# Optimization experiments

Hardware: AMD Instinct MI355X
Metric: run time of the kernel (lower is better)

## Reference

```python
import jax, jax.numpy as jnp
import numpy as np

B, T, D, H = 8, 1024, 768, 12
HD = D // H  # head_dim = 64


def setup_inputs() -> dict:
    key = jax.random.key(0)
    ks = jax.random.split(key, 6)
    s = 1.0 / np.sqrt(D)
    return {
        "x": jax.random.normal(ks[0], (B, T, D), dtype=jnp.float32),
        "Wq": jax.random.normal(ks[1], (D, D), dtype=jnp.float32) * s,
        "Wk": jax.random.normal(ks[2], (D, D), dtype=jnp.float32) * s,
        "Wv": jax.random.normal(ks[3], (D, D), dtype=jnp.float32) * s,
        "Wp": jax.random.normal(ks[4], (D, D), dtype=jnp.float32) * s,
        "bp": jnp.zeros((D,), dtype=jnp.float32),
    }


def reference(x, Wq, Wk, Wv, Wp, bp):
    Bx, Tx, Dx = x.shape
    # projections (nn.Linear applies x @ W.T; weights here are stored as [out,in]-equivalent square)
    q = (x @ Wq.T).reshape(Bx, Tx, H, HD).transpose(0, 2, 1, 3)  # [B,H,T,hd]
    k = (x @ Wk.T).reshape(Bx, Tx, H, HD).transpose(0, 2, 1, 3)
    v = (x @ Wv.T).reshape(Bx, Tx, H, HD).transpose(0, 2, 1, 3)
    scores = jnp.einsum("bhqd,bhkd->bhqk", q, k)  # raw QK^T, then mask, then scale (as in source)
    causal = jnp.tril(jnp.ones((Tx, Tx), dtype=bool))
    scores = jnp.where(causal, scores, -jnp.inf)
    weights = jax.nn.softmax(scores / np.sqrt(HD), axis=-1)
    # dropout is identity in eval mode
    ctx = jnp.einsum("bhqk,bhkd->bhqd", weights, v)
    ctx = ctx.transpose(0, 2, 1, 3).reshape(Bx, Tx, Dx)
    return ctx @ Wp.T + bp
```

## Files before the change

### kernel.cpp

```cpp
#include <hip/hip_runtime.h>
#include <hip/hip_bf16.h>
#include <math.h>

#define Bsz 8
#define Tsz 1024
#define Dsz 768
#define Hn  12
#define Msz (Bsz*Tsz)
#define NQT (Tsz/64)

typedef __attribute__((ext_vector_type(8))) short bf16x8_t;
typedef __attribute__((ext_vector_type(4))) float f32x4_t;

__device__ __forceinline__ unsigned short f2bf(float f) {
  unsigned u = __builtin_bit_cast(unsigned, f);
  u += 0x7FFFu + ((u >> 16) & 1u);
  return (unsigned short)(u >> 16);
}

__device__ __forceinline__ unsigned short f2bf_fast(float f) {
  __hip_bfloat16 h = __float2bfloat16(f);
  return __builtin_bit_cast(unsigned short, h);
}

__device__ __forceinline__ void gload16(const void* g, const void* l) {
  __builtin_amdgcn_global_load_lds(
      (const __attribute__((address_space(1))) unsigned int*)g,
      (__attribute__((address_space(3))) unsigned int*)l, 16, 0, 0);
}

#define XBLKS (Msz*Dsz/1024)
#define WBLKS (Dsz*Dsz/1024)
__global__ __launch_bounds__(256) void cvt_all_kernel(
    const float* __restrict__ x,
    const float* __restrict__ w0, const float* __restrict__ w1,
    const float* __restrict__ w2, const float* __restrict__ w3,
    unsigned short* __restrict__ xb,
    unsigned short* __restrict__ o0, unsigned short* __restrict__ o1,
    unsigned short* __restrict__ o2, unsigned short* __restrict__ o3) {
  int bid = blockIdx.x;
  const float* src; unsigned short* dst; size_t blk;
  if (bid < XBLKS) { src = x; dst = xb; blk = bid; }
  else {
    int t = bid - XBLKS;
    int which = t / WBLKS;
    blk = t % WBLKS;
    switch (which) {
      case 0: src = w0; dst = o0; break;
      case 1: src = w1; dst = o1; break;
      case 2: src = w2; dst = o2; break;
      default: src = w3; dst = o3; break;
    }
  }
  size_t idx = (blk * 256 + threadIdx.x) * 4;
  float4 v = *(const float4*)(src + idx);
  union { unsigned short u[4]; uint2 w; } t;
  t.u[0] = f2bf(v.x); t.u[1] = f2bf(v.y); t.u[2] = f2bf(v.z); t.u[3] = f2bf(v.w);
  *(uint2*)(dst + idx) = t.w;
}

__global__ __launch_bounds__(256) void gemm_qkv_kernel(
    const unsigned short* __restrict__ X, const unsigned short* __restrict__ Wcat,
    unsigned short* __restrict__ Yq, unsigned short* __restrict__ Yk,
    unsigned short* __restrict__ Yvt) {
  __shared__ __align__(16) unsigned short As[128 * 64];
  __shared__ __align__(16) unsigned short Bs[128 * 64];
  const int tid = threadIdx.x;
  const int w = tid >> 6, lane = tid & 63;
  const int i = lane & 15, g = lane >> 4;
  const int wr = w >> 1, wc = w & 1;
  const int bm = blockIdx.x * 128, bn = blockIdx.y * 128;
  const int sr = lane >> 3;
  const int scb = ((lane & 7) * 16) ^ (sr << 4);

  f32x4_t acc[4][4];
  #pragma unroll
  for (int a = 0; a < 4; ++a)
    #pragma unroll
    for (int b2 = 0; b2 < 4; ++b2)
      #pragma unroll
      for (int r = 0; r < 4; ++r) acc[a][b2][r] = 0.f;

  for (int k0 = 0; k0 < Dsz; k0 += 64) {
    __syncthreads();
    #pragma unroll
    for (int j = 0; j < 4; ++j) {
      const int c = 4 * w + j;
      const int row = 8 * c + sr;
      gload16((const char*)X + ((size_t)(bm + row) * Dsz + k0) * 2 + scb,
              (const char*)As + c * 1024);
      gload16((const char*)Wcat + ((size_t)(bn + row) * Dsz + k0) * 2 + scb,
              (const char*)Bs + c * 1024);
    }
    __syncthreads();
    bf16x8_t af[4][2];
    #pragma unroll
    for (int f = 0; f < 4; ++f) {
      const int R = 64 * wr + 16 * f + i;
      #pragma unroll
      for (int kk = 0; kk < 2; ++kk)
        af[f][kk] = *(const bf16x8_t*)((const char*)As + R * 128 +
                                       ((64 * kk + 16 * g) ^ ((i & 7) << 4)));
    }
    #pragma unroll
    for (int b2 = 0; b2 < 4; ++b2) {
      const int R = 64 * wc + 16 * b2 + i;
      const bf16x8_t b0 = *(const bf16x8_t*)((const char*)Bs + R * 128 +
                                             ((16 * g) ^ ((i & 7) << 4)));
      const bf16x8_t b1 = *(const bf16x8_t*)((const char*)Bs + R * 128 +
                                             ((64 + 16 * g) ^ ((i & 7) << 4)));
      #pragma unroll
      for (int a = 0; a < 4; ++a) {
        acc[a][b2] = __builtin_amdgcn_mfma_f32_16x16x32_bf16(af[a][0], b0, acc[a][b2], 0, 0, 0);
        acc[a][b2] = __builtin_amdgcn_mfma_f32_16x16x32_bf16(af[a][1], b1, acc[a][b2], 0, 0, 0);
      }
    }
  }

  const int wsel = blockIdx.y / 6;
  const int nloc = (blockIdx.y % 6) * 128;
  if (wsel < 2) {
    unsigned short* Y = wsel ? Yk : Yq;
    const float sc = wsel ? 1.0f : 0.18033688f;
    #pragma unroll
    for (int fi = 0; fi < 4; ++fi)
      #pragma unroll
      for (int fj = 0; fj < 4; ++fj) {
        const int n = nloc + 64 * wc + 16 * fj + i;
        #pragma unroll
        for (int r = 0; r < 4; ++r) {
          const int m = bm + 64 * wr + 16 * fi + 4 * g + r;
          Y[(size_t)m * Dsz + n] = f2bf_fast(acc[fi][fj][r] * sc);
        }
      }
  } else {
    #pragma unroll
    for (int fi = 0; fi < 4; ++fi)
      #pragma unroll
      for (int fj = 0; fj < 4; ++fj) {
        const int m0 = bm + 64 * wr + 16 * fi + 4 * g;
        const int bb = m0 >> 10;
        const int t  = m0 & 1023;
        const int n  = nloc + 64 * wc + 16 * fj + i;
        union { unsigned short u[4]; uint2 v; } pk;
        #pragma unroll
        for (int r = 0; r < 4; ++r) pk.u[r] = f2bf_fast(acc[fi][fj][r]);
        *(uint2*)&Yvt[((size_t)(bb * Dsz + n)) * Tsz + t] = pk.v;
      }
  }
}

__global__ __launch_bounds__(256) void gemm_proj_kernel(
    const unsigned short* __restrict__ X, const unsigned short* __restrict__ W,
    const float* __restrict__ bias, float* __restrict__ Y) {
  __shared__ __align__(16) unsigned short As[128 * 64];
  __shared__ __align__(16) unsigned short Bs[128 * 64];
  const int tid = threadIdx.x;
  const int w = tid >> 6, lane = tid & 63;
  const int i = lane & 15, g = lane >> 4;
  const int wr = w >> 1, wc = w & 1;
  const int bm = blockIdx.x * 128, bn = blockIdx.y * 128;
  const int sr = lane >> 3;
  const int scb = ((lane & 7) * 16) ^ (sr << 4);

  f32x4_t acc[4][4];
  #pragma unroll
  for (int a = 0; a < 4; ++a)
    #pragma unroll
    for (int b2 = 0; b2 < 4; ++b2)
      #pragma unroll
      for (int r = 0; r < 4; ++r) acc[a][b2][r] = 0.f;

  for (int k0 = 0; k0 < Dsz; k0 += 64) {
    __syncthreads();
    #pragma unroll
    for (int j = 0; j < 4; ++j) {
      const int c = 4 * w + j;
      const int row = 8 * c + sr;
      gload16((const char*)X + ((size_t)(bm + row) * Dsz + k0) * 2 + scb,
              (const char*)As + c * 1024);
      gload16((const char*)W + ((size_t)(bn + row) * Dsz + k0) * 2 + scb,
              (const char*)Bs + c * 1024);
    }
    __syncthreads();
    bf16x8_t af[4][2];
    #pragma unroll
    for (int f = 0; f < 4; ++f) {
      const int R = 64 * wr + 16 * f + i;
      #pragma unroll
      for (int kk = 0; kk < 2; ++kk)
        af[f][kk] = *(const bf16x8_t*)((const char*)As + R * 128 +
                                       ((64 * kk + 16 * g) ^ ((i & 7) << 4)));
    }
    #pragma unroll
    for (int b2 = 0; b2 < 4; ++b2) {
      const int R = 64 * wc + 16 * b2 + i;
      const bf16x8_t b0 = *(const bf16x8_t*)((const char*)Bs + R * 128 +
                                             ((16 * g) ^ ((i & 7) << 4)));
      const bf16x8_t b1 = *(const bf16x8_t*)((const char*)Bs + R * 128 +
                                             ((64 + 16 * g) ^ ((i & 7) << 4)));
      #pragma unroll
      for (int a = 0; a < 4; ++a) {
        acc[a][b2] = __builtin_amdgcn_mfma_f32_16x16x32_bf16(af[a][0], b0, acc[a][b2], 0, 0, 0);
        acc[a][b2] = __builtin_amdgcn_mfma_f32_16x16x32_bf16(af[a][1], b1, acc[a][b2], 0, 0, 0);
      }
    }
  }

  #pragma unroll
  for (int fi = 0; fi < 4; ++fi)
    #pragma unroll
    for (int fj = 0; fj < 4; ++fj) {
      const int n = bn + 64 * wc + 16 * fj + i;
      const float bv = bias[n];
      #pragma unroll
      for (int r = 0; r < 4; ++r) {
        const int m = bm + 64 * wr + 16 * fi + 4 * g + r;
        Y[(size_t)m * Dsz + n] = acc[fi][fj][r] + bv;
      }
    }
}

__global__ __launch_bounds__(512) void attn_mfma_kernel(
    const unsigned short* __restrict__ Qm, const unsigned short* __restrict__ Km,
    const unsigned short* __restrict__ Vt, unsigned short* __restrict__ ctx) {
  __shared__ __align__(16) unsigned short Ks[2][64 * 64];
  __shared__ __align__(16) unsigned short Vs[2][64 * 64];
  __shared__ __align__(16) unsigned short Ps[8][16 * 72];
  const int tid = threadIdx.x, w = tid >> 6, lane = tid & 63;
  const int i = lane & 15, g = lane >> 4;
  const int grp = w >> 2, wl = w & 3;
  const int bh = blockIdx.x, b = bh / Hn, h = bh % Hn;
  const int j = blockIdx.y;
  const int qt = 2 * j + grp;
  const int t0 = qt * 64;
  const int ntB = 2 * j + 2;

  const int sr  = lane >> 3;
  const int swz = ((lane & 7) * 16) ^ (sr << 4);

  bf16x8_t qa[2];
  {
    const unsigned short* qp =
        Qm + ((size_t)(b * Tsz + t0 + 16 * wl + i) * Dsz + h * 64 + 8 * g);
    qa[0] = *(const bf16x8_t*)qp;
    qa[1] = *(const bf16x8_t*)(qp + 32);
  }

  f32x4_t o[4];
  #pragma unroll
  for (int fd = 0; fd < 4; ++fd)
    #pragma unroll
    for (int r = 0; r < 4; ++r) o[fd][r] = 0.f;
  float mrun[4] = {-3.0e38f, -3.0e38f, -3.0e38f, -3.0e38f};
  float lrun[4] = {0.f, 0.f, 0.f, 0.f};

  auto STAGE = [&](int kv0, int p) {
    const int row = 8 * w + sr;
    gload16((const char*)Km + ((size_t)(b * Tsz + kv0 + row) * Dsz + h * 64) * 2 + swz,
            (const char*)Ks[p] + w * 1024);
    gload16((const char*)Vt + ((size_t)(bh * 64 + row) * Tsz + kv0) * 2 + swz,
            (const char*)Vs[p] + w * 1024);
  };

  STAGE(0, 0);
  unsigned short* Pw = &Ps[w][0];

  for (int kt = 0; kt < ntB; ++kt) {
    const int p = kt & 1;
    __syncthreads();
    if (kt + 1 < ntB) STAGE((kt + 1) * 64, p ^ 1);

    if (kt <= qt) {
      f32x4_t s[4];
      __builtin_amdgcn_s_setprio(1);
      #pragma unroll
      for (int fj = 0; fj < 4; ++fj) {
        #pragma unroll
        for (int r = 0; r < 4; ++r) s[fj][r] = 0.f;
        const int R = 16 * fj + i;
        #pragma unroll
        for (int ks = 0; ks < 2; ++ks) {
          const bf16x8_t kb = *(const bf16x8_t*)((const char*)Ks[p] + R * 128 +
                                                 ((64 * ks + 16 * g) ^ ((i & 7) << 4)));
          s[fj] = __builtin_amdgcn_mfma_f32_16x16x32_bf16(qa[ks], kb, s[fj], 0, 0, 0);
        }
      }
      __builtin_amdgcn_s_setprio(0);

      if (kt == qt) {
        #pragma unroll
        for (int fj = 0; fj < 4; ++fj) {
          const int kidx = kt * 64 + 16 * fj + i;
          #pragma unroll
          for (int r = 0; r < 4; ++r)
            if (kidx > t0 + 16 * wl + 4 * g + r) s[fj][r] = -1.0e30f;
        }
      }

      float mx[4];
      #pragma unroll
      for (int r = 0; r < 4; ++r)
        mx[r] = fmaxf(fmaxf(s[0][r], s[1][r]), fmaxf(s[2][r], s[3][r]));
      #pragma unroll
      for (int r = 0; r < 4; ++r) {
        mx[r] = fmaxf(mx[r], __shfl_xor(mx[r], 1));
        mx[r] = fmaxf(mx[r], __shfl_xor(mx[r], 2));
        mx[r] = fmaxf(mx[r], __shfl_xor(mx[r], 4));
        mx[r] = fmaxf(mx[r], __shfl_xor(mx[r], 8));
      }

      bool nd = false;
      #pragma unroll
      for (int r = 0; r < 4; ++r) nd = nd || (mx[r] > mrun[r] + 8.0f);
      if (__any(nd)) {
        #pragma unroll
        for (int r = 0; r < 4; ++r) {
          const float mn = fmaxf(mrun[r], mx[r]);
          const float fs = exp2f(mrun[r] - mn);
          mrun[r] = mn;
          lrun[r] *= fs;
          #pragma unroll
          for (int fd = 0; fd < 4; ++fd) o[fd][r] *= fs;
        }
      }

      float rs[4] = {0.f, 0.f, 0.f, 0.f};
      #pragma unroll
      for (int fj = 0; fj < 4; ++fj)
        #pragma unroll
        for (int r = 0; r < 4; ++r) {
          s[fj][r] = exp2f(s[fj][r] - mrun[r]);
          rs[r] += s[fj][r];
        }
      #pragma unroll
      for (int r = 0; r < 4; ++r) {
        rs[r] += __shfl_xor(rs[r], 1);
        rs[r] += __shfl_xor(rs[r], 2);
        rs[r] += __shfl_xor(rs[r], 4);
        rs[r] += __shfl_xor(rs[r], 8);
        lrun[r] += rs[r];
      }

      #pragma unroll
      for (int fj = 0; fj < 4; ++fj)
        #pragma unroll
        for (int r = 0; r < 4; ++r)
          Pw[(4 * g + r) * 72 + 16 * fj + i] = f2bf_fast(s[fj][r]);

      __builtin_amdgcn_s_setprio(1);
      #pragma unroll
      for (int ks = 0; ks < 2; ++ks) {
        const bf16x8_t pa = *(const bf16x8_t*)&Pw[i * 72 + 32 * ks + 8 * g];
        #pragma unroll
        for (int fd = 0; fd < 4; ++fd) {
          const int R = 16 * fd + i;
          const bf16x8_t vb = *(const bf16x8_t*)((const char*)Vs[p] + R * 128 +
                                                 ((64 * ks + 16 * g) ^ ((i & 7) << 4)));
          o[fd] = __builtin_amdgcn_mfma_f32_16x16x32_bf16(pa, vb, o[fd], 0, 0, 0);
        }
      }
      __builtin_amdgcn_s_setprio(0);
    }
  }

  #pragma unroll
  for (int r = 0; r < 4; ++r) {
    const float inv = 1.f / lrun[r];
    const int qidx = t0 + 16 * wl + 4 * g + r;
    #pragma unroll
    for (int fd = 0; fd < 4; ++fd)
      ctx[(size_t)(b * Tsz + qidx) * Dsz + h * 64 + 16 * fd + i] =
          f2bf_fast(o[fd][r] * inv);
  }
}

extern "C" void kernel_launch(void* const* d_in, const int* in_sizes, int n_in,
                              void* d_out, int out_size, void* d_ws, size_t ws_size,
                              hipStream_t stream) {
  const float* x  = (const float*)d_in[0];
  const float* Wq = (const float*)d_in[1];
  const float* Wk = (const float*)d_in[2];
  const float* Wv = (const float*)d_in[3];
  const float* Wp = (const float*)d_in[4];
  const float* bp = (const float*)d_in[5];
  float* out = (float*)d_out;

  const size_t md = (size_t)Msz * Dsz;
  const size_t wd = (size_t)Dsz * Dsz;
  unsigned short* xb   = (unsigned short*)d_ws;
  unsigned short* wqb  = xb + md;
  unsigned short* wkb  = wqb + wd;
  unsigned short* wvb  = wkb + wd;
  unsigned short* wpb  = wvb + wd;
  unsigned short* qb   = wpb + wd;
  unsigned short* kb   = qb + md;
  unsigned short* vtb  = kb + md;
  unsigned short* ctxb = vtb + md;

  cvt_all_kernel<<<XBLKS + 4 * WBLKS, 256, 0, stream>>>(
      x, Wq, Wk, Wv, Wp, xb, wqb, wkb, wvb, wpb);

  gemm_qkv_kernel<<<dim3(Msz / 128, 18), 256, 0, stream>>>(xb, wqb, qb, kb, vtb);

  attn_mfma_kernel<<<dim3(Bsz * Hn, 8), 512, 0, stream>>>(qb, kb, vtb, ctxb);

  gemm_proj_kernel<<<dim3(Msz / 128, Dsz / 128), 256, 0, stream>>>(ctxb, wpb, bp, out);
}
```

Before: 211.4 us.

## Balance causal attention blocks by pairing tiles and use DPP reductions

Each block now pairs query tile j with tile NQT-1-j, so every block processes the same number of KV tiles. This removes the load imbalance of the causal triangle. Row-max reductions switch from ds_swizzle/shfl to DPP row operations. The row-sum reduction is deferred to the epilogue by keeping per-lane partial sums.

```diff
diff --git a/kernel.cpp b/kernel.cpp
--- a/kernel.cpp
+++ b/kernel.cpp
@@ -11,6 +11,9 @@
 
 typedef __attribute__((ext_vector_type(8))) short bf16x8_t;
 typedef __attribute__((ext_vector_type(4))) float f32x4_t;
+
+#define DPPF(v, CTRL) __builtin_bit_cast(float, __builtin_amdgcn_update_dpp( \
+    0, __builtin_bit_cast(int, (v)), (CTRL), 0xF, 0xF, true))
 
 __device__ __forceinline__ unsigned short f2bf(float f) {
   unsigned u = __builtin_bit_cast(unsigned, f);
@@ -232,9 +235,9 @@
   const int grp = w >> 2, wl = w & 3;
   const int bh = blockIdx.x, b = bh / Hn, h = bh % Hn;
   const int j = blockIdx.y;
-  const int qt = 2 * j + grp;
+  const int qt = grp ? (NQT - 1 - j) : j;
   const int t0 = qt * 64;
-  const int ntB = 2 * j + 2;
+  const int nkt = NQT - j;
 
   const int sr  = lane >> 3;
   const int swz = ((lane & 7) * 16) ^ (sr << 4);
@@ -266,10 +269,10 @@
   STAGE(0, 0);
   unsigned short* Pw = &Ps[w][0];
 
-  for (int kt = 0; kt < ntB; ++kt) {
+  for (int kt = 0; kt < nkt; ++kt) {
     const int p = kt & 1;
     __syncthreads();
-    if (kt + 1 < ntB) STAGE((kt + 1) * 64, p ^ 1);
+    if (kt + 1 < nkt) STAGE((kt + 1) * 64, p ^ 1);
 
     if (kt <= qt) {
       f32x4_t s[4];
@@ -300,14 +303,13 @@
 
       float mx[4];
       #pragma unroll
-      for (int r = 0; r < 4; ++r)
-        mx[r] = fmaxf(fmaxf(s[0][r], s[1][r]), fmaxf(s[2][r], s[3][r]));
-      #pragma unroll
       for (int r = 0; r < 4; ++r) {
-        mx[r] = fmaxf(mx[r], __shfl_xor(mx[r], 1));
-        mx[r] = fmaxf(mx[r], __shfl_xor(mx[r], 2));
-        mx[r] = fmaxf(mx[r], __shfl_xor(mx[r], 4));
-        mx[r] = fmaxf(mx[r], __shfl_xor(mx[r], 8));
+        float v = fmaxf(fmaxf(s[0][r], s[1][r]), fmaxf(s[2][r], s[3][r]));
+        v = fmaxf(v, DPPF(v, 0xB1));
+        v = fmaxf(v, DPPF(v, 0x4E));
+        v = fmaxf(v, DPPF(v, 0x141));
+        v = fmaxf(v, DPPF(v, 0x140));
+        mx[r] = v;
       }
 
       bool nd = false;
@@ -325,22 +327,13 @@
         }
       }
 
-      float rs[4] = {0.f, 0.f, 0.f, 0.f};
       #pragma unroll
       for (int fj = 0; fj < 4; ++fj)
         #pragma unroll
         for (int r = 0; r < 4; ++r) {
           s[fj][r] = exp2f(s[fj][r] - mrun[r]);
-          rs[r] += s[fj][r];
-        }
-      #pragma unroll
-      for (int r = 0; r < 4; ++r) {
-        rs[r] += __shfl_xor(rs[r], 1);
-        rs[r] += __shfl_xor(rs[r], 2);
-        rs[r] += __shfl_xor(rs[r], 4);
-        rs[r] += __shfl_xor(rs[r], 8);
-        lrun[r] += rs[r];
-      }
+          lrun[r] += s[fj][r];
+        }
 
       #pragma unroll
       for (int fj = 0; fj < 4; ++fj)
@@ -366,7 +359,12 @@
 
   #pragma unroll
   for (int r = 0; r < 4; ++r) {
-    const float inv = 1.f / lrun[r];
+    float l = lrun[r];
+    l += DPPF(l, 0xB1);
+    l += DPPF(l, 0x4E);
+    l += DPPF(l, 0x141);
+    l += DPPF(l, 0x140);
+    const float inv = 1.f / l;
     const int qidx = t0 + 16 * wl + 4 * g + r;
     #pragma unroll
     for (int fd = 0; fd < 4; ++fd)
```

New measurement: 202.2 us. 1.05x faster.
